# Optimization experiments

Measured on AMD Instinct MI355X. Metric: run time of the kernel, lower is better.

Reference implementation:

```python
import jax, jax.numpy as jnp
import numpy as np

N, D, E, H, O, K = 4096, 1024, 8, 4096, 1024, 2
LOSS_COEF = 0.01


def setup_inputs() -> dict:
    key = jax.random.key(0)
    ks = jax.random.split(key, 4)
    scale = lambda k, shape, fan: (jax.random.normal(k, shape, jnp.float32) / np.sqrt(fan).astype(np.float32))
    return {
        "x": jax.random.normal(ks[0], (N, D), jnp.float32),
        "Wg": scale(ks[1], (D, E), D),            # gating network
        "W1": scale(ks[2], (E, D, H), D),          # stacked expert layer 1
        "b1": jnp.zeros((E, H), jnp.float32),
        "W2": scale(ks[3], (E, H, O), H),          # stacked expert layer 2
        "b2": jnp.zeros((E, O), jnp.float32),
        "k": K,
    }


def _cv_squared(v):
    # coefficient-of-variation squared, the tensor2tensor load-balancing loss
    eps = jnp.asarray(1e-10, v.dtype)
    m = jnp.mean(v)
    return jnp.var(v) / (m * m + eps)


def reference(x, Wg, W1, b1, W2, b2, k):
    n, e = x.shape[0], Wg.shape[1]
    # --- top-k gating (deterministic / inference path) ---
    logits = x @ Wg                               # [N, E]
    top_vals, top_idx = jax.lax.top_k(logits, k)  # [N, k]
    top_gates = jax.nn.softmax(top_vals, axis=-1)
    gates = jnp.zeros((n, e), x.dtype).at[jnp.arange(n)[:, None], top_idx].set(top_gates)  # [N, E], sparse rows
    # --- expert compute (dense grouped form of dispatch->expert->combine) ---
    h = jax.nn.relu(jnp.einsum('nd,edh->enh', x, W1) + b1[:, None, :])  # [E, N, H]
    y = jnp.einsum('enh,eho->eno', h, W2) + b2[:, None, :]               # [E, N, O]
    out = jnp.einsum('ne,eno->no', gates, y)                              # weighted combine [N, O]
    # --- auxiliary load-balancing loss ---
    importance = gates.sum(axis=0)                # [E]
    aux_loss = LOSS_COEF * _cv_squared(importance)
    return out, aux_loss
```

## Files before the change

### kernel.cpp

```cpp
#include <hip/hip_runtime.h>
#include <hip/hip_bf16.h>
#include <stdint.h>

#define N_TOK 4096
#define DIM   1024
#define NE    8
#define HID   4096
#define OUTD  1024
#define TOPK  2
#define SLOTS (N_TOK*TOPK)
#define MAXT0 640
#define MAXT1 320

typedef __bf16 bf16_t;
typedef __attribute__((ext_vector_type(8))) __bf16 bf16x8;
typedef __attribute__((ext_vector_type(4))) __bf16 bf16x4;
typedef __attribute__((ext_vector_type(4))) float  f32x4;

__global__ __launch_bounds__(512)
void k_prep(const float* __restrict__ x,  const float* __restrict__ wg,
            const float* __restrict__ w1, const float* __restrict__ w2,
            bf16_t* __restrict__ xb, bf16_t* __restrict__ w1t, bf16_t* __restrict__ w2t,
            int* __restrict__ tki, float* __restrict__ tkg) {
    __shared__ bf16_t tT[128][264];
    const int bx = blockIdx.x;
    const int t  = threadIdx.x;
    if (bx < 2048) {
        const float* src; bf16_t* dst; int R, C, ry, cx;
        if (bx < 1024) {
            int e = bx >> 7, rem = bx & 127;
            ry = rem >> 5; cx = rem & 31;
            src = w1 + (size_t)e * DIM * HID; dst = w1t + (size_t)e * DIM * HID;
            R = DIM; C = HID;
        } else {
            int b2 = bx - 1024;
            int e = b2 >> 7, rem = b2 & 127;
            ry = rem >> 3; cx = rem & 7;
            src = w2 + (size_t)e * HID * OUTD; dst = w2t + (size_t)e * HID * OUTD;
            R = HID; C = OUTD;
        }
        const int r0 = ry * 256, c0 = cx * 128;
        const int tx = t & 31;
        const int ro = t >> 5;
#pragma unroll
        for (int p = 0; p < 2; ++p) {
            int rblk = 128 * p + 8 * ro;
            float4 va[8];
#pragma unroll
            for (int u = 0; u < 8; ++u)
                va[u] = *(const float4*)&src[(size_t)(r0 + rblk + u) * C + c0 + tx * 4];
#pragma unroll
            for (int j = 0; j < 4; ++j) {
                bf16x8 o;
#pragma unroll
                for (int u = 0; u < 8; ++u) o[u] = (__bf16)((&va[u].x)[j]);
                *(bf16x8*)&tT[tx * 4 + j][rblk] = o;
            }
        }
        __syncthreads();
        const int w = t >> 6, l = t & 63;
        const int ccb = w * 2 + (l >> 5);
        const int rb  = (l & 31) * 8;
#pragma unroll
        for (int q = 0; q < 8; ++q) {
            int cc = q * 16 + ccb;
            bf16x8 o = *(const bf16x8*)&tT[cc][rb];
            *(bf16x8*)&dst[(size_t)(c0 + cc) * R + r0 + rb] = o;
        }
        return;
    }
    int n = (bx - 2048) * 8 + (t >> 6);
    int lane = t & 63;
    const float* xr = x + (size_t)n * DIM;
    double acc[NE];
#pragma unroll
    for (int e = 0; e < NE; ++e) acc[e] = 0.0;
#pragma unroll
    for (int i = 0; i < 4; ++i) {
        int d0 = i * 256 + lane * 4;
        float4 v = *(const float4*)&xr[d0];
        bf16x4 o;
        o[0] = (__bf16)v.x; o[1] = (__bf16)v.y; o[2] = (__bf16)v.z; o[3] = (__bf16)v.w;
        *(bf16x4*)&xb[(size_t)n * DIM + d0] = o;
        const float* wr = wg + (size_t)d0 * NE;
#pragma unroll
        for (int j = 0; j < 4; ++j) {
            double xv = (double)((&v.x)[j]);
#pragma unroll
            for (int e = 0; e < NE; ++e) acc[e] += xv * (double)wr[j * NE + e];
        }
    }
#pragma unroll
    for (int e = 0; e < NE; ++e)
        for (int off = 32; off > 0; off >>= 1) acc[e] += __shfl_xor(acc[e], off);
    if (lane == 0) {
        int i0 = 0; double v0 = acc[0];
#pragma unroll
        for (int e = 1; e < NE; ++e) if (acc[e] > v0) { v0 = acc[e]; i0 = e; }
        int i1 = -1; double v1 = -1e300;
#pragma unroll
        for (int e = 0; e < NE; ++e) if (e != i0 && acc[e] > v1) { v1 = acc[e]; i1 = e; }
        double e1 = exp(v1 - v0);
        double s = 1.0 + e1;
        tki[n*2]   = i0;  tki[n*2+1] = i1;
        tkg[n*2]   = (float)(1.0 / s);
        tkg[n*2+1] = (float)(e1 / s);
    }
}

__global__ __launch_bounds__(256)
void k_route(const int* __restrict__ tki, const float* __restrict__ tkg,
             int* __restrict__ counts, int* __restrict__ bases,
             int* __restrict__ tb0, int* __restrict__ tb1,
             float* __restrict__ aux_out,
             int* __restrict__ tok_ids, int* __restrict__ slotmap) {
    const int e = blockIdx.x, t = threadIdx.x;
    const int wid = t >> 6, lane = t & 63;
    int   lc[NE]; float lg[NE];
#pragma unroll
    for (int k = 0; k < NE; ++k) { lc[k] = 0; lg[k] = 0.f; }
    for (int i = t; i < SLOTS; i += 256) {
        int ee = tki[i]; float gg = tkg[i];
#pragma unroll
        for (int k = 0; k < NE; ++k) if (ee == k) { lc[k]++; lg[k] += gg; }
    }
#pragma unroll
    for (int k = 0; k < NE; ++k)
        for (int off = 32; off > 0; off >>= 1) {
            lc[k] += __shfl_xor(lc[k], off);
            lg[k] += __shfl_xor(lg[k], off);
        }
    __shared__ int   wcI[4][NE];
    __shared__ float wcF[4][NE];
    if (lane == 0)
#pragma unroll
        for (int k = 0; k < NE; ++k) { wcI[wid][k] = lc[k]; wcF[wid][k] = lg[k]; }
    __syncthreads();
    int cnt[NE];
#pragma unroll
    for (int k = 0; k < NE; ++k)
        cnt[k] = wcI[0][k] + wcI[1][k] + wcI[2][k] + wcI[3][k];
    if (e == 0 && t == 0) {
        float gs[NE];
#pragma unroll
        for (int k = 0; k < NE; ++k)
            gs[k] = wcF[0][k] + wcF[1][k] + wcF[2][k] + wcF[3][k];
        float m = 0.f;
        for (int k = 0; k < NE; ++k) m += gs[k];
        m /= (float)NE;
        float var = 0.f;
        for (int k = 0; k < NE; ++k) { float d = gs[k] - m; var += d * d; }
        var /= (float)NE;
        aux_out[0] = 0.01f * var / (m * m + 1e-10f);
        int b = 0, c0 = 0, c1 = 0;
        tb0[0] = 0; tb1[0] = 0;
        for (int k = 0; k < NE; ++k) {
            counts[k] = cnt[k]; bases[k] = b; b += cnt[k];
            int nty = (cnt[k] + 255) >> 8;
            c0 += 16 * nty; c1 += 8 * nty;
            tb0[k+1] = c0; tb1[k+1] = c1;
        }
    }
    int run = 0;
    for (int k = 0; k < e; ++k) run += cnt[k];
    __shared__ int wc[4];
    for (int base = 0; base < SLOTS; base += 256) {
        int i = base + t;
        bool f = (tki[i] == e);
        unsigned long long bl = __ballot(f);
        int pre = __popcll(bl & ((1ull << lane) - 1ull));
        if (lane == 0) wc[wid] = __popcll(bl);
        __syncthreads();
        int woff = 0;
#pragma unroll
        for (int u = 0; u < 4; ++u) if (u < wid) woff += wc[u];
        int tot = wc[0] + wc[1] + wc[2] + wc[3];
        if (f) { int s = run + woff + pre; tok_ids[s] = i >> 1; slotmap[i] = s; }
        run += tot;
        __syncthreads();
    }
}

template <int MODE>
__global__ __launch_bounds__(512, 2)
void k_gemm(const bf16_t* __restrict__ A,
            const bf16_t* __restrict__ Bt,
            const float* __restrict__ bias,
            const int* __restrict__ tok_ids,
            const int* __restrict__ bases,
            const int* __restrict__ counts,
            const int* __restrict__ tb,
            bf16_t* __restrict__ Y) {
    constexpr int KD   = (MODE == 0) ? DIM : HID;
    constexpr int ND   = (MODE == 0) ? HID : OUTD;
    constexpr int KLEN = (MODE == 0) ? DIM : (HID / 2);
    constexpr int KT   = KLEN / 32;
    constexpr int BUFE = 16384;

    const int ti = blockIdx.x;
    if (ti >= tb[NE]) return;
    int e = 0;
#pragma unroll
    for (int k = 1; k < NE; ++k) if (ti >= tb[k]) e = k;
    const int local = ti - tb[e];
    const int ne = counts[e];
    const int b0 = bases[e];
    int panel, y, kslot = 0;
    if (MODE == 0) { y = local >> 4; panel = local & 15; }
    else           { y = local >> 3; int q = local & 7; panel = q >> 1; kslot = q & 1; }
    const int m0 = y * 256, n0 = panel * 256;
    const int koff = (MODE == 0) ? 0 : kslot * KLEN;
    bf16_t* __restrict__ Yw = (MODE == 0) ? Y : (Y + (size_t)kslot * SLOTS * OUTD);

    extern __shared__ bf16_t lds[];

    const int t = threadIdx.x, w = t >> 6, L = t & 63;
    const int wm = w >> 2, wn = w & 3;
    const int lr = L & 15, lq = L >> 4;
    const int srow  = L >> 2;
    const int sslot = L & 3;

    int offA[8], offB[4];
#pragma unroll
    for (int i = 0; i < 8; ++i) {
        int r = wm * 128 + i * 16 + lr;
        offA[i] = r * 32 + ((lq ^ ((r >> 1) & 3)) << 3);
    }
#pragma unroll
    for (int j = 0; j < 4; ++j) {
        int r = wn * 64 + j * 16 + lr;
        offB[j] = 8192 + r * 32 + ((lq ^ ((r >> 1) & 3)) << 3);
    }
    int sdstA[2], sdstB[2];
#pragma unroll
    for (int g = 0; g < 2; ++g) {
        sdstA[g] = (g * 128 + w * 16) * 32;
        sdstB[g] = 8192 + (g * 128 + w * 16) * 32;
    }

#define GLL(srcp, dste) __builtin_amdgcn_global_load_lds( \
        (const __attribute__((address_space(1))) uint32_t*)(srcp), \
        (__attribute__((address_space(3))) uint32_t*)(lds + (dste)), 16, 0, 0)
#define STAGE(Tt, bsl) { \
        _Pragma("unroll") for (int g_ = 0; g_ < 2; ++g_) { \
            GLL(aptr[g_] + (Tt) * 32, (bsl) * BUFE + sdstA[g_]); \
            GLL(bptr[g_] + (Tt) * 32, (bsl) * BUFE + sdstB[g_]); } }

    const bf16_t* aptr[2];
    const bf16_t* bptr[2];
#pragma unroll
    for (int g = 0; g < 2; ++g) {
        int row = g * 128 + w * 16 + srow;
        int gk  = sslot ^ ((row >> 1) & 3);
        int mm = m0 + row;
        int rr = (mm < ne) ? mm : (ne - 1);
        size_t arow = (MODE == 0) ? (size_t)tok_ids[b0 + rr] * KD : (size_t)(b0 + rr) * KD;
        aptr[g] = A + arow + koff + gk * 8;
        bptr[g] = Bt + ((size_t)e * ND + n0 + row) * KD + koff + gk * 8;
    }

    f32x4 acc[8][4];
#pragma unroll
    for (int i = 0; i < 8; ++i)
#pragma unroll
        for (int j = 0; j < 4; ++j) acc[i][j] = (f32x4){0.f, 0.f, 0.f, 0.f};

    STAGE(0, 0); STAGE(1, 1);

    int cb = 0;
    int nb = 2;
    for (int T = 0; T < KT; ++T) {
        if (T < KT - 1) { asm volatile("s_waitcnt vmcnt(4)" ::: "memory"); }
        else            { asm volatile("s_waitcnt vmcnt(0)" ::: "memory"); }
        __builtin_amdgcn_s_barrier();
        if (T + 2 < KT) STAGE(T + 2, nb);

        bf16x8 fb[4], fa[8];
#pragma unroll
        for (int j = 0; j < 4; ++j) fb[j] = *(const bf16x8*)(lds + cb * BUFE + offB[j]);
#pragma unroll
        for (int i = 0; i < 4; ++i) fa[i] = *(const bf16x8*)(lds + cb * BUFE + offA[i]);
        __builtin_amdgcn_sched_barrier(0);
#pragma unroll
        for (int i = 4; i < 8; ++i) fa[i] = *(const bf16x8*)(lds + cb * BUFE + offA[i]);
        __builtin_amdgcn_sched_barrier(0);
        asm volatile("s_waitcnt lgkmcnt(4)" ::: "memory");
        __builtin_amdgcn_sched_barrier(0);
        __builtin_amdgcn_s_setprio(1);
#pragma unroll
        for (int i = 0; i < 4; ++i)
#pragma unroll
            for (int j = 0; j < 4; ++j)
                acc[i][j] = __builtin_amdgcn_mfma_f32_16x16x32_bf16(fb[j], fa[i], acc[i][j], 0, 0, 0);
        __builtin_amdgcn_s_setprio(0);
        asm volatile("s_waitcnt lgkmcnt(0)" ::: "memory");
        __builtin_amdgcn_sched_barrier(0);
        __builtin_amdgcn_s_setprio(1);
#pragma unroll
        for (int i = 4; i < 8; ++i)
#pragma unroll
            for (int j = 0; j < 4; ++j)
                acc[i][j] = __builtin_amdgcn_mfma_f32_16x16x32_bf16(fb[j], fa[i], acc[i][j], 0, 0, 0);
        __builtin_amdgcn_s_setprio(0);

        cb = (cb == 2) ? 0 : cb + 1;
        nb = (nb == 2) ? 0 : nb + 1;
    }

    const int kbias = (MODE == 0) ? 1 : (kslot == 0 ? 1 : 0);
#pragma unroll
    for (int i = 0; i < 8; ++i) {
        int gm = m0 + wm * 128 + i * 16 + lr;
        if (gm < ne) {
#pragma unroll
            for (int j = 0; j < 4; ++j) {
                int gn = n0 + wn * 64 + j * 16 + lq * 4;
                f32x4 bv = *(const f32x4*)&bias[(size_t)e * ND + gn];
                bf16x4 hv;
#pragma unroll
                for (int r = 0; r < 4; ++r) {
                    float v = acc[i][j][r];
                    if (kbias) v += bv[r];
                    if (MODE == 0) v = fmaxf(v, 0.f);
                    hv[r] = (__bf16)v;
                }
                *(bf16x4*)&Yw[(size_t)(b0 + gm) * ND + gn] = hv;
            }
        }
    }
#undef STAGE
#undef GLL
}

__global__ void k_combine(const bf16_t* __restrict__ ybuf,
                          const int* __restrict__ slotmap,
                          const float* __restrict__ tkg,
                          float* __restrict__ out) {
    int n = blockIdx.x;
    int d = threadIdx.x * 4;
    int s0 = slotmap[2 * n], s1 = slotmap[2 * n + 1];
    float g0 = tkg[2 * n],  g1 = tkg[2 * n + 1];
    const bf16_t* y2 = ybuf + (size_t)SLOTS * OUTD;
    bf16x4 a0 = *(const bf16x4*)&ybuf[(size_t)s0 * OUTD + d];
    bf16x4 a1 = *(const bf16x4*)&y2  [(size_t)s0 * OUTD + d];
    bf16x4 c0 = *(const bf16x4*)&ybuf[(size_t)s1 * OUTD + d];
    bf16x4 c1 = *(const bf16x4*)&y2  [(size_t)s1 * OUTD + d];
    f32x4 o;
#pragma unroll
    for (int r = 0; r < 4; ++r)
        o[r] = g0 * ((float)a0[r] + (float)a1[r]) + g1 * ((float)c0[r] + (float)c1[r]);
    *(f32x4*)&out[(size_t)n * OUTD + d] = o;
}

extern "C" void kernel_launch(void* const* d_in, const int* in_sizes, int n_in,
                              void* d_out, int out_size, void* d_ws, size_t ws_size,
                              hipStream_t stream) {
    const float* x  = (const float*)d_in[0];
    const float* wg = (const float*)d_in[1];
    const float* w1 = (const float*)d_in[2];
    const float* b1 = (const float*)d_in[3];
    const float* w2 = (const float*)d_in[4];
    const float* b2 = (const float*)d_in[5];
    float* out = (float*)d_out;

    char* ws = (char*)d_ws;
    size_t o = 0;
    auto alloc = [&](size_t b) { size_t r = o; o = (o + b + 255) & ~(size_t)255; return r; };
    int*    counts  = (int*)(ws + alloc(NE * 4));
    int*    bases   = (int*)(ws + alloc(NE * 4));
    int*    tb0     = (int*)(ws + alloc((NE + 1) * 4));
    int*    tb1     = (int*)(ws + alloc((NE + 1) * 4));
    int*    tki     = (int*)(ws + alloc(SLOTS * 4));
    float*  tkg     = (float*)(ws + alloc(SLOTS * 4));
    int*    tok_ids = (int*)(ws + alloc(SLOTS * 4));
    int*    slotmap = (int*)(ws + alloc(SLOTS * 4));
    bf16_t* xb      = (bf16_t*)(ws + alloc((size_t)N_TOK * DIM * 2));
    size_t  w1t_off = alloc((size_t)NE * HID * DIM * 2);
    bf16_t* w1t     = (bf16_t*)(ws + w1t_off);
    bf16_t* ybuf    = (bf16_t*)(ws + w1t_off);
    bf16_t* w2t     = (bf16_t*)(ws + alloc((size_t)NE * OUTD * HID * 2));
    bf16_t* hbuf    = (bf16_t*)(ws + alloc((size_t)SLOTS * HID * 2));
    (void)ws_size; (void)n_in; (void)in_sizes;

    hipFuncSetAttribute((const void*)&k_gemm<0>, hipFuncAttributeMaxDynamicSharedMemorySize, 98304);
    hipFuncSetAttribute((const void*)&k_gemm<1>, hipFuncAttributeMaxDynamicSharedMemorySize, 98304);

    k_prep<<<2048 + 512, 512, 0, stream>>>(x, wg, w1, w2, xb, w1t, w2t, tki, tkg);
    k_route<<<NE, 256, 0, stream>>>(tki, tkg, counts, bases, tb0, tb1,
                                    out + (size_t)N_TOK * OUTD, tok_ids, slotmap);

    k_gemm<0><<<MAXT0, 512, 98304, stream>>>(xb, w1t, b1, tok_ids, bases, counts, tb0, hbuf);
    k_gemm<1><<<MAXT1, 512, 98304, stream>>>(hbuf, w2t, b2, tok_ids, bases, counts, tb1, ybuf);

    k_combine<<<N_TOK, 256, 0, stream>>>(ybuf, slotmap, tkg, out);
}
```

Baseline: 334.4 us.

## Move W2 transpose-convert into first expert GEMM launch to overlap with compute

The fp32-to-bf16 transpose of W2 moves out of the prep kernel and into extra trailing blocks of the first grouped GEMM launch. Those blocks reuse the dynamic LDS buffer as the staging tile and exit early. W2 conversion is then no longer on the critical path before routing and the first GEMM, and its memory traffic can fill idle CUs while GEMM tiles run. The risk is that the extra blocks compete for CU slots and bandwidth with the GEMM tiles, or are scheduled only after them.

```diff
diff --git a/kernel.cpp b/kernel.cpp
--- a/kernel.cpp
+++ b/kernel.cpp
@@ -11,65 +11,62 @@
 #define SLOTS (N_TOK*TOPK)
 #define MAXT0 640
 #define MAXT1 320
+#define W2TB  1024
 
 typedef __bf16 bf16_t;
 typedef __attribute__((ext_vector_type(8))) __bf16 bf16x8;
 typedef __attribute__((ext_vector_type(4))) __bf16 bf16x4;
 typedef __attribute__((ext_vector_type(4))) float  f32x4;
 
+static __device__ __forceinline__ void tr_tile(const float* __restrict__ src,
+                                               bf16_t* __restrict__ dst,
+                                               int R, int C, int ry, int cx,
+                                               bf16_t (*tT)[264], int t) {
+    const int r0 = ry * 256, c0 = cx * 128;
+    const int tx = t & 31;
+    const int ro = t >> 5;
+#pragma unroll
+    for (int p = 0; p < 2; ++p) {
+        int rblk = 128 * p + 8 * ro;
+        float4 va[8];
+#pragma unroll
+        for (int u = 0; u < 8; ++u)
+            va[u] = *(const float4*)&src[(size_t)(r0 + rblk + u) * C + c0 + tx * 4];
+#pragma unroll
+        for (int j = 0; j < 4; ++j) {
+            bf16x8 o;
+#pragma unroll
+            for (int u = 0; u < 8; ++u) o[u] = (__bf16)((&va[u].x)[j]);
+            *(bf16x8*)&tT[tx * 4 + j][rblk] = o;
+        }
+    }
+    __syncthreads();
+    const int w = t >> 6, l = t & 63;
+    const int ccb = w * 2 + (l >> 5);
+    const int rb  = (l & 31) * 8;
+#pragma unroll
+    for (int q = 0; q < 8; ++q) {
+        int cc = q * 16 + ccb;
+        bf16x8 o = *(const bf16x8*)&tT[cc][rb];
+        *(bf16x8*)&dst[(size_t)(c0 + cc) * R + r0 + rb] = o;
+    }
+}
+
 __global__ __launch_bounds__(512)
 void k_prep(const float* __restrict__ x,  const float* __restrict__ wg,
-            const float* __restrict__ w1, const float* __restrict__ w2,
-            bf16_t* __restrict__ xb, bf16_t* __restrict__ w1t, bf16_t* __restrict__ w2t,
+            const float* __restrict__ w1,
+            bf16_t* __restrict__ xb, bf16_t* __restrict__ w1t,
             int* __restrict__ tki, float* __restrict__ tkg) {
     __shared__ bf16_t tT[128][264];
     const int bx = blockIdx.x;
     const int t  = threadIdx.x;
-    if (bx < 2048) {
-        const float* src; bf16_t* dst; int R, C, ry, cx;
-        if (bx < 1024) {
-            int e = bx >> 7, rem = bx & 127;
-            ry = rem >> 5; cx = rem & 31;
-            src = w1 + (size_t)e * DIM * HID; dst = w1t + (size_t)e * DIM * HID;
-            R = DIM; C = HID;
-        } else {
-            int b2 = bx - 1024;
-            int e = b2 >> 7, rem = b2 & 127;
-            ry = rem >> 3; cx = rem & 7;
-            src = w2 + (size_t)e * HID * OUTD; dst = w2t + (size_t)e * HID * OUTD;
-            R = HID; C = OUTD;
-        }
-        const int r0 = ry * 256, c0 = cx * 128;
-        const int tx = t & 31;
-        const int ro = t >> 5;
-#pragma unroll
-        for (int p = 0; p < 2; ++p) {
-            int rblk = 128 * p + 8 * ro;
-            float4 va[8];
-#pragma unroll
-            for (int u = 0; u < 8; ++u)
-                va[u] = *(const float4*)&src[(size_t)(r0 + rblk + u) * C + c0 + tx * 4];
-#pragma unroll
-            for (int j = 0; j < 4; ++j) {
-                bf16x8 o;
-#pragma unroll
-                for (int u = 0; u < 8; ++u) o[u] = (__bf16)((&va[u].x)[j]);
-                *(bf16x8*)&tT[tx * 4 + j][rblk] = o;
-            }
-        }
-        __syncthreads();
-        const int w = t >> 6, l = t & 63;
-        const int ccb = w * 2 + (l >> 5);
-        const int rb  = (l & 31) * 8;
-#pragma unroll
-        for (int q = 0; q < 8; ++q) {
-            int cc = q * 16 + ccb;
-            bf16x8 o = *(const bf16x8*)&tT[cc][rb];
-            *(bf16x8*)&dst[(size_t)(c0 + cc) * R + r0 + rb] = o;
-        }
+    if (bx < 1024) {
+        int e = bx >> 7, rem = bx & 127;
+        tr_tile(w1 + (size_t)e * DIM * HID, w1t + (size_t)e * DIM * HID,
+                DIM, HID, rem >> 5, rem & 31, tT, t);
         return;
     }
-    int n = (bx - 2048) * 8 + (t >> 6);
+    int n = (bx - 1024) * 8 + (t >> 6);
     int lane = t & 63;
     const float* xr = x + (size_t)n * DIM;
     double acc[NE];
@@ -190,12 +187,25 @@
             const int* __restrict__ bases,
             const int* __restrict__ counts,
             const int* __restrict__ tb,
+            const float* __restrict__ w2,
+            bf16_t* __restrict__ w2t,
             bf16_t* __restrict__ Y) {
     constexpr int KD   = (MODE == 0) ? DIM : HID;
     constexpr int ND   = (MODE == 0) ? HID : OUTD;
     constexpr int KLEN = (MODE == 0) ? DIM : (HID / 2);
     constexpr int KT   = KLEN / 32;
     constexpr int BUFE = 16384;
+
+    extern __shared__ bf16_t lds[];
+
+    if (MODE == 0 && blockIdx.x >= MAXT0) {
+        int b2 = blockIdx.x - MAXT0;
+        int e = b2 >> 7, rem = b2 & 127;
+        tr_tile(w2 + (size_t)e * HID * OUTD, w2t + (size_t)e * HID * OUTD,
+                HID, OUTD, rem >> 3, rem & 7,
+                (bf16_t(*)[264])lds, threadIdx.x);
+        return;
+    }
 
     const int ti = blockIdx.x;
     if (ti >= tb[NE]) return;
@@ -211,8 +221,6 @@
     const int m0 = y * 256, n0 = panel * 256;
     const int koff = (MODE == 0) ? 0 : kslot * KLEN;
     bf16_t* __restrict__ Yw = (MODE == 0) ? Y : (Y + (size_t)kslot * SLOTS * OUTD);
-
-    extern __shared__ bf16_t lds[];
 
     const int t = threadIdx.x, w = t >> 6, L = t & 63;
     const int wm = w >> 2, wn = w & 3;
@@ -385,12 +393,14 @@
     hipFuncSetAttribute((const void*)&k_gemm<0>, hipFuncAttributeMaxDynamicSharedMemorySize, 98304);
     hipFuncSetAttribute((const void*)&k_gemm<1>, hipFuncAttributeMaxDynamicSharedMemorySize, 98304);
 
-    k_prep<<<2048 + 512, 512, 0, stream>>>(x, wg, w1, w2, xb, w1t, w2t, tki, tkg);
+    k_prep<<<1024 + 512, 512, 0, stream>>>(x, wg, w1, xb, w1t, tki, tkg);
     k_route<<<NE, 256, 0, stream>>>(tki, tkg, counts, bases, tb0, tb1,
                                     out + (size_t)N_TOK * OUTD, tok_ids, slotmap);
 
-    k_gemm<0><<<MAXT0, 512, 98304, stream>>>(xb, w1t, b1, tok_ids, bases, counts, tb0, hbuf);
-    k_gemm<1><<<MAXT1, 512, 98304, stream>>>(hbuf, w2t, b2, tok_ids, bases, counts, tb1, ybuf);
+    k_gemm<0><<<MAXT0 + W2TB, 512, 98304, stream>>>(
+        xb, w1t, b1, tok_ids, bases, counts, tb0, w2, w2t, hbuf);
+    k_gemm<1><<<MAXT1, 512, 98304, stream>>>(
+        hbuf, w2t, b2, tok_ids, bases, counts, tb1, nullptr, nullptr, ybuf);
 
     k_combine<<<N_TOK, 256, 0, stream>>>(ybuf, slotmap, tkg, out);
 }
```

Result: faster. 312.8 us (-6.5%).
